# Optimization experiments

Hardware: AMD Instinct MI355X
Metric: run time of the kernel (lower is better)

## Reference

```python
import jax, jax.numpy as jnp
import numpy as np

L, H, M, KB = 8, 512, 32, 256  # layers, hidden, fourier modes, key bits
EPS = 1e-5


def setup_inputs() -> dict:
    key = jax.random.key(0)
    ks = jax.random.split(key, 20)
    B, S = 8, 2048
    s = 0.02
    return {
        'x': jax.random.normal(ks[0], (B, S), jnp.float32),
        # input projection Linear(1, H): weight [H] (squeezed), bias [H]
        'in_w': jax.random.normal(ks[1], (H,), jnp.float32) * s,
        'in_b': jax.random.normal(ks[2], (H,), jnp.float32) * s,
        # per-layer fourier weights (complex, stored as real/imag), conv1d(k=1), layernorm
        'fw_r': jax.random.normal(ks[3], (L, M, H, H), jnp.float32) * s,
        'fw_i': jax.random.normal(ks[4], (L, M, H, H), jnp.float32) * s,
        'conv_w': jax.random.normal(ks[5], (L, H, H), jnp.float32) / np.sqrt(H),
        'conv_b': jax.random.normal(ks[6], (L, H), jnp.float32) * s,
        'ln_g': jnp.ones((L, H), jnp.float32),
        'ln_b': jnp.zeros((L, H), jnp.float32),
        # output projection H -> H/2 -> H/4 -> 1
        'op1_w': jax.random.normal(ks[7], (H // 2, H), jnp.float32) / np.sqrt(H),
        'op1_b': jnp.zeros((H // 2,), jnp.float32),
        'op2_w': jax.random.normal(ks[8], (H // 4, H // 2), jnp.float32) / np.sqrt(H // 2),
        'op2_b': jnp.zeros((H // 4,), jnp.float32),
        'op3_w': jax.random.normal(ks[9], (1, H // 4), jnp.float32) / np.sqrt(H // 4),
        'op3_b': jnp.zeros((1,), jnp.float32),
        # cryptanalytic head H -> H -> KB (sigmoid)
        'h1_w': jax.random.normal(ks[10], (H, H), jnp.float32) / np.sqrt(H),
        'h1_b': jnp.zeros((H,), jnp.float32),
        'h2_w': jax.random.normal(ks[11], (KB, H), jnp.float32) / np.sqrt(H),
        'h2_b': jnp.zeros((KB,), jnp.float32),
    }


def _gelu(x):
    return jax.nn.gelu(x, approximate=False)


def _fourier_layer(x, Wc, cw, cb, g, b):
    # x: [B, S, H]; Wc: [M, H, H] complex
    S = x.shape[1]
    x_ft = jnp.fft.rfft(x, axis=1)  # [B, F, H] complex, F = S//2+1
    m = min(M, x_ft.shape[1])
    # batched per-mode complex GEMM (replaces python loop over modes)
    spec = jnp.einsum('bmh,mhk->bmk', x_ft[:, :m], Wc[:m])
    out_ft = jnp.concatenate([spec, jnp.zeros_like(x_ft[:, m:])], axis=1)
    x_fourier = jnp.fft.irfft(out_ft, n=S, axis=1)  # real [B, S, H]
    x_conv = x @ cw.T + cb  # Conv1d kernel-size-1 == per-position linear
    y = x_fourier + x_conv
    mu = jnp.mean(y, axis=-1, keepdims=True)
    var = jnp.var(y, axis=-1, keepdims=True)
    return (y - mu) * jax.lax.rsqrt(var + EPS) * g + b


def reference(x, in_w, in_b, fw_r, fw_i, conv_w, conv_b, ln_g, ln_b,
              op1_w, op1_b, op2_w, op2_b, op3_w, op3_b,
              h1_w, h1_b, h2_w, h2_b):
    # input projection: Linear(1, H) on x[..., None]
    h = x[:, :, None] * in_w[None, None, :] + in_b  # [B, S, H]
    Wc = fw_r + 1j * fw_i  # [L, M, H, H]
    for l in range(L):
        h = _fourier_layer(h, Wc[l], conv_w[l], conv_b[l], ln_g[l], ln_b[l]) + h
    # output projection (dropout is identity in eval)
    o = _gelu(h @ op1_w.T + op1_b)
    o = _gelu(o @ op2_w.T + op2_b)
    output = (o @ op3_w.T + op3_b)[..., 0]  # [B, S]
    gf = jnp.mean(h, axis=1)  # [B, H]
    k = _gelu(gf @ h1_w.T + h1_b)
    key_pred = jax.nn.sigmoid(k @ h2_w.T + h2_b)  # [B, KB]
    return output, key_pred
```

## Files before the change

### kernel.cpp

```cpp
#include <hip/hip_runtime.h>
#include <hip/hip_bf16.h>
#include <math.h>

#define BB   8
#define SEQ  2048
#define HD   512
#define LAY  8
#define MD   32
#define NKB  256
#define LNEPS 1e-5f

typedef __attribute__((ext_vector_type(8))) short v8s;
typedef __attribute__((ext_vector_type(4))) float v4f;
typedef __attribute__((ext_vector_type(4))) unsigned short v4us;

__device__ __forceinline__ float b2f(__hip_bfloat16 v) { return __bfloat162float(v); }
__device__ __forceinline__ float geluf(float v) { return v * 0.5f * (1.f + erff(v * 0.70710678118654752f)); }
__device__ __forceinline__ float bflo(unsigned int u) { return __uint_as_float((u & 0xFFFFu) << 16); }
__device__ __forceinline__ float bfhi(unsigned int u) { return __uint_as_float(u & 0xFFFF0000u); }

__device__ __forceinline__ float ldin(const void* p, size_t i, int bf) {
    if (bf) return __bfloat162float(((const __hip_bfloat16*)p)[i]);
    return ((const float*)p)[i];
}
__device__ __forceinline__ void stout(void* p, size_t i, float v, int bf) {
    if (bf) ((__hip_bfloat16*)p)[i] = __float2bfloat16(v);
    else    ((float*)p)[i] = v;
}

__device__ __forceinline__ void gl2lds16(const void* g, void* l) {
    __builtin_amdgcn_global_load_lds((__attribute__((address_space(1))) void*)g,
                                     (__attribute__((address_space(3))) void*)l, 16, 0, 0);
}

__device__ __forceinline__ unsigned short f2bfu(float f) {
    __hip_bfloat16 b = __float2bfloat16(f);
    return *(unsigned short*)&b;
}

__global__ void k_flag(const unsigned int* __restrict__ lng_bits, int* __restrict__ flag) {
    if (threadIdx.x == 0 && blockIdx.x == 0)
        *flag = (lng_bits[0] == 0x3F803F80u) ? 1 : 0;
}

__global__ void k_setup(const void* __restrict__ x, const void* __restrict__ in_w, const void* __restrict__ in_b,
                        const void* __restrict__ cw, const void* __restrict__ w1, const void* __restrict__ w2,
                        const void* __restrict__ h1w, const void* __restrict__ h2w,
                        __hip_bfloat16* __restrict__ Ffwd, __hip_bfloat16* __restrict__ T2,
                        __hip_bfloat16* __restrict__ cwbf, __hip_bfloat16* __restrict__ w1bf,
                        __hip_bfloat16* __restrict__ w2bf, float* __restrict__ h1T, float* __restrict__ h2T,
                        float* __restrict__ h,
                        float* __restrict__ gf,
                        const int* __restrict__ flag) {
    int bf = *flag;
    int blk = blockIdx.x, t = threadIdx.x;
    if (blk < 512) {
        int idx = blk * 256 + t;
        int j = idx >> 11, s = idx & 2047;
        int m = j >> 1;
        int phase = (m * s) & (SEQ - 1);
        float ang = (float)phase * (6.283185307179586f / (float)SEQ);
        Ffwd[idx] = __float2bfloat16((j & 1) ? -sinf(ang) : cosf(ang));
    } else if (blk < 1024) {
        int idx = (blk - 512) * 256 + t;
        int s = idx >> 6, j = idx & 63;
        int m = j >> 1;
        float v;
        if (j == 0)      v = 1.f / (float)SEQ;
        else if (j == 1) v = 0.f;
        else {
            int phase = (m * s) & (SEQ - 1);
            float ang = (float)phase * (6.283185307179586f / (float)SEQ);
            v = (j & 1) ? (-2.f / (float)SEQ) * sinf(ang) : (2.f / (float)SEQ) * cosf(ang);
        }
        T2[idx] = __float2bfloat16(v);
    } else if (blk < 9216) {
        int idx = (blk - 1024) * 256 + t;
        cwbf[idx] = __float2bfloat16(ldin(cw, idx, bf));
    } else if (blk < 9728) {
        int idx = (blk - 9216) * 256 + t;
        w1bf[idx] = __float2bfloat16(ldin(w1, idx, bf));
    } else if (blk < 9856) {
        int idx = (blk - 9728) * 256 + t;
        w2bf[idx] = __float2bfloat16(ldin(w2, idx, bf));
    } else if (blk < 10880) {
        int idx = (blk - 9856) * 256 + t;
        int r = idx & 511, c = idx >> 9;
        h1T[idx] = ldin(h1w, (size_t)r * 512 + c, bf);
    } else if (blk < 11392) {
        int idx = (blk - 10880) * 256 + t;
        int r = idx & 255, c = idx >> 8;
        h2T[idx] = ldin(h2w, (size_t)r * 512 + c, bf);
    } else if (blk < 11408) {
        int idx = (blk - 11392) * 256 + t;
        gf[idx] = 0.f;
    } else {
        int idx = (blk - 11408) * 256 + t;
        int j = idx & 511;
        int bs = idx >> 9;
        float v = ldin(x, bs, bf) * ldin(in_w, j, bf) + ldin(in_b, j, bf);
        h[idx] = v;
    }
}

__global__ __launch_bounds__(256) void k_fdft2(const float* __restrict__ h,
                                               const __hip_bfloat16* __restrict__ Ffwd,
                                               float* __restrict__ Xpart) {
    __shared__ __align__(16) __hip_bfloat16 Als[2][16 * 72];
    int t = threadIdx.x;
    int lane = t & 63, wv = t >> 6;
    int ln15 = lane & 15, quad = lane >> 4;
    int ht = blockIdx.x, b = blockIdx.y, kh = blockIdx.z;
    int kcs = kh * 16;
    int sr = t >> 2, hc = (t & 3) * 4;

    v4f acc = (v4f){0.f, 0.f, 0.f, 0.f};

    const float* asrc0 = h + (size_t)b * SEQ * HD + ht * 16;
    const __hip_bfloat16* fbase = Ffwd + (size_t)(wv * 16 + ln15) * SEQ + quad * 8;

    float4 cur = *(const float4*)(asrc0 + (size_t)(kcs * 64 + sr) * HD + hc);
    {
        const float* cf = (const float*)&cur;
#pragma unroll
        for (int e = 0; e < 4; e++)
            Als[0][(hc + e) * 72 + sr] = __float2bfloat16(cf[e]);
    }
    __syncthreads();
    for (int i = 0; i < 16; i++) {
        int buf = i & 1;
        float4 nxt = cur;
        if (i < 15)
            nxt = *(const float4*)(asrc0 + (size_t)((kcs + i + 1) * 64 + sr) * HD + hc);
        v8s bf0 = *(const v8s*)(fbase + (kcs + i) * 64);
        v8s bf1 = *(const v8s*)(fbase + (kcs + i) * 64 + 32);
        v8s af0 = *(const v8s*)&Als[buf][ln15 * 72 + quad * 8];
        v8s af1 = *(const v8s*)&Als[buf][ln15 * 72 + 32 + quad * 8];
        acc = __builtin_amdgcn_mfma_f32_16x16x32_bf16(af0, bf0, acc, 0, 0, 0);
        acc = __builtin_amdgcn_mfma_f32_16x16x32_bf16(af1, bf1, acc, 0, 0, 0);
        if (i < 15) {
            const float* nf = (const float*)&nxt;
#pragma unroll
            for (int e = 0; e < 4; e++)
                Als[buf ^ 1][(hc + e) * 72 + sr] = __float2bfloat16(nf[e]);
        }
        __syncthreads();
        cur = nxt;
    }
    int j = wv * 16 + ln15;
    int m = j >> 1, c = j & 1;
    int hg = ht * 16 + quad * 4;
    float* outp = Xpart + (size_t)kh * 262144 + (size_t)(b * 32 + m) * 1024;
#pragma unroll
    for (int r = 0; r < 4; r++)
        outp[(size_t)(hg + r) * 2 + c] = acc[r];
}

__global__ __launch_bounds__(512) void k_mix(const float* __restrict__ Xp0, const float* __restrict__ Xp1,
                                             const void* __restrict__ fwr, const void* __restrict__ fwi,
                                             __hip_bfloat16* __restrict__ spec2, int l,
                                             const int* __restrict__ flag) {
    int bf = *flag;
    int kt = blockIdx.x;
    int m  = blockIdx.y;
    int t = threadIdx.x;
    int kl = t & 15, hg = t >> 4;
    int k0 = kt * 64 + kl * 4;
    __shared__ float xs[8192];
    __shared__ float red[32 * 512];
    for (int e = t; e < 8192; e += 512) {
        int bb = e >> 10, r = e & 1023;
        size_t off = (size_t)(bb * 32 + m) * 1024 + r;
        xs[bb * 1024 + r] = Xp0[off] + Xp1[off];
    }
    __syncthreads();
    float ar[8][4], ai[8][4];
#pragma unroll
    for (int bb = 0; bb < 8; bb++)
#pragma unroll
        for (int q = 0; q < 4; q++) { ar[bb][q] = 0.f; ai[bb][q] = 0.f; }
    size_t wbase = (size_t)(l * 32 + m) * 262144 + k0;
    const float2* xs2 = (const float2*)xs;
    if (bf) {
        const __hip_bfloat16* fr = (const __hip_bfloat16*)fwr;
        const __hip_bfloat16* fi = (const __hip_bfloat16*)fwi;
#pragma unroll 2
        for (int hh = hg; hh < 512; hh += 32) {
            v4us urv = *(const v4us*)(fr + wbase + (size_t)hh * 512);
            v4us uiv = *(const v4us*)(fi + wbase + (size_t)hh * 512);
            float wr[4], wi[4];
#pragma unroll
            for (int q = 0; q < 4; q++) {
                wr[q] = __uint_as_float(((unsigned int)(unsigned short)urv[q]) << 16);
                wi[q] = __uint_as_float(((unsigned int)(unsigned short)uiv[q]) << 16);
            }
#pragma unroll
            for (int bb = 0; bb < 8; bb++) {
                float2 x2 = xs2[bb * 512 + hh];
#pragma unroll
                for (int q = 0; q < 4; q++) {
                    ar[bb][q] += x2.x * wr[q] - x2.y * wi[q];
                    ai[bb][q] += x2.x * wi[q] + x2.y * wr[q];
                }
            }
        }
    } else {
        const float* fr = (const float*)fwr;
        const float* fi = (const float*)fwi;
#pragma unroll 2
        for (int hh = hg; hh < 512; hh += 32) {
            v4f wrv = *(const v4f*)(fr + wbase + (size_t)hh * 512);
            v4f wiv = *(const v4f*)(fi + wbase + (size_t)hh * 512);
#pragma unroll
            for (int bb = 0; bb < 8; bb++) {
                float2 x2 = xs2[bb * 512 + hh];
#pragma unroll
                for (int q = 0; q < 4; q++) {
                    ar[bb][q] += x2.x * wrv[q] - x2.y * wiv[q];
                    ai[bb][q] += x2.x * wiv[q] + x2.y * wrv[q];
                }
            }
        }
    }
    v4f* red4 = (v4f*)red;
#pragma unroll
    for (int bb = 0; bb < 8; bb++)
        red4[hg * 128 + bb * 16 + kl] = (v4f){ar[bb][0], ar[bb][1], ar[bb][2], ar[bb][3]};
    __syncthreads();
    float sr = 0.f;
#pragma unroll
    for (int g = 0; g < 32; g++) sr += red[g * 512 + t];
    __syncthreads();
#pragma unroll
    for (int bb = 0; bb < 8; bb++)
        red4[hg * 128 + bb * 16 + kl] = (v4f){ai[bb][0], ai[bb][1], ai[bb][2], ai[bb][3]};
    __syncthreads();
    float si = 0.f;
#pragma unroll
    for (int g = 0; g < 32; g++) si += red[g * 512 + t];

    int bb = t >> 6, j = t & 63;
    int k = kt * 64 + j;
    size_t o = ((size_t)(bb * 512 + k) << 6) + 2 * m;
    __hip_bfloat16 hr = __float2bfloat16(sr), hi = __float2bfloat16(si);
    unsigned int pk = (unsigned int)*(unsigned short*)&hr | ((unsigned int)*(unsigned short*)&hi << 16);
    *(unsigned int*)(spec2 + o) = pk;
}

__global__ __launch_bounds__(512) void k_gln(__hip_bfloat16* __restrict__ hbf,
                                             const __hip_bfloat16* __restrict__ cwbf,
                                             const __hip_bfloat16* __restrict__ T2,
                                             const __hip_bfloat16* __restrict__ spec2,
                                             const void* __restrict__ cb,
                                             const void* __restrict__ lng, const void* __restrict__ lnb,
                                             float* __restrict__ h,
                                             int l, const int* __restrict__ flag) {
    int bfv = *flag;
    __shared__ __align__(16) __hip_bfloat16 smem[2][19456];
    __shared__ float stats[128];
    __hip_bfloat16* Yls = &smem[0][0];

    int t = threadIdx.x;
    int lane = t & 63, wv = t >> 6;
    int wr = wv >> 2, wc = wv & 3;
    int ln15 = lane & 15, quad = lane >> 4;
    int row0 = blockIdx.x * 64;
    int b = row0 >> 11, s0 = row0 & 2047;
    int arow = t >> 3, acolq = (t & 7) * 4;

    v4f acc[16];
#pragma unroll
    for (int i = 0; i < 16; i++) acc[i] = (v4f){0.f, 0.f, 0.f, 0.f};

    const __hip_bfloat16* cwl = cwbf + (size_t)l * 262144;

    auto stageB = [&](int buf, int kc) {
        int k0 = kc * 32;
#pragma unroll
        for (int p = 0; p < 4; p++) {
            int i = p * 512 + t;
            int n = i >> 2, kq = (i & 3) * 8;
            const __hip_bfloat16* bsrc = (k0 < 512)
                ? cwl + (size_t)n * 512 + k0 + kq
                : spec2 + (size_t)(b * 512 + n) * 64 + (k0 - 512) + kq;
            gl2lds16(bsrc, &smem[buf][2560 + (size_t)(p * 512 + wv * 64) * 8]);
        }
    };
    auto loadA = [&](int kc, float4& av, v4us& tv) {
        int k0 = kc * 32;
        if (k0 < 512) {
            av = *(const float4*)&h[(size_t)(row0 + arow) * HD + k0 + acolq];
        } else {
            tv = *(const v4us*)&T2[(size_t)(s0 + arow) * 64 + (k0 - 512) + acolq];
        }
    };
    auto writeA = [&](int buf, int kc, const float4& av, const v4us& tv) {
        __hip_bfloat16* dst = &smem[buf][arow * 40 + acolq];
        if (kc * 32 < 512) {
            const float* af = (const float*)&av;
            v4us pk;
#pragma unroll
            for (int e = 0; e < 4; e++) pk[e] = (short)f2bfu(af[e]);
            *(v4us*)dst = pk;
        } else {
            *(v4us*)dst = tv;
        }
    };

    {
        float4 av; v4us tv;
        loadA(0, av, tv);
        stageB(0, 0);
        writeA(0, 0, av, tv);
    }
    __syncthreads();
    int cur = 0;
    float4 avn; v4us tvn;
    for (int kc = 0; kc < 18; kc++) {
        if (kc < 17) {
            loadA(kc + 1, avn, tvn);
            stageB(cur ^ 1, kc + 1);
        }
        const __hip_bfloat16* Als = &smem[cur][0];
        const __hip_bfloat16* Bls = &smem[cur][2560];
        v8s af[2], bfr[8];
#pragma unroll
        for (int i = 0; i < 2; i++)
            af[i] = *(const v8s*)&Als[(wr * 32 + i * 16 + ln15) * 40 + quad * 8];
#pragma unroll
        for (int j = 0; j < 8; j++)
            bfr[j] = *(const v8s*)&Bls[(wc * 128 + j * 16 + ln15) * 32 + quad * 8];
#pragma unroll
        for (int i = 0; i < 2; i++)
#pragma unroll
            for (int j = 0; j < 8; j++)
                acc[i * 8 + j] = __builtin_amdgcn_mfma_f32_16x16x32_bf16(af[i], bfr[j], acc[i * 8 + j], 0, 0, 0);
        if (kc < 17) writeA(cur ^ 1, kc + 1, avn, tvn);
        __syncthreads();
        cur ^= 1;
    }
#pragma unroll
    for (int j = 0; j < 8; j++) {
        int col = wc * 128 + j * 16 + ln15;
        float cbv = ldin(cb, l * HD + col, bfv);
#pragma unroll
        for (int i = 0; i < 2; i++) {
            int rl = wr * 32 + i * 16 + quad * 4;
#pragma unroll
            for (int r = 0; r < 4; r++)
                Yls[(rl + r) * 520 + col] = __float2bfloat16(acc[i * 8 + j][r] + cbv);
        }
    }
    __syncthreads();
    {
        int r = t >> 3, g2 = t & 7;
        float s = 0.f, q = 0.f;
        for (int i = 0; i < 32; i++) {
            int cp = g2 + i * 8;
            unsigned int u = *(const unsigned int*)&Yls[r * 520 + cp * 2];
            float v0 = bflo(u), v1 = bfhi(u);
            s += v0 + v1; q += v0 * v0 + v1 * v1;
        }
        s += __shfl_xor(s, 1); s += __shfl_xor(s, 2); s += __shfl_xor(s, 4);
        q += __shfl_xor(q, 1); q += __shfl_xor(q, 2); q += __shfl_xor(q, 4);
        if (g2 == 0) {
            float mu = s * (1.f / (float)HD);
            float var = q * (1.f / (float)HD) - mu * mu;
            stats[r * 2] = mu; stats[r * 2 + 1] = rsqrtf(var + LNEPS);
        }
    }
    __syncthreads();
    {
        int c2 = t & 255;
        int gc = 2 * c2;
        float g0 = ldin(lng, l * HD + gc, bfv),     g1 = ldin(lng, l * HD + gc + 1, bfv);
        float b0 = ldin(lnb, l * HD + gc, bfv),     b1 = ldin(lnb, l * HD + gc + 1, bfv);
        int rbase = t >> 8;
        int last = (l == LAY - 1);
        for (int k = 0; k < 32; k++) {
            int r = rbase + 2 * k;
            float mu = stats[r * 2], rs = stats[r * 2 + 1];
            unsigned int u = *(const unsigned int*)&Yls[r * 520 + c2 * 2];
            float v0 = bflo(u), v1 = bfhi(u);
            float2 hv = *(const float2*)&h[(size_t)(row0 + r) * HD + gc];
            float n0 = (v0 - mu) * rs * g0 + b0 + hv.x;
            float n1 = (v1 - mu) * rs * g1 + b1 + hv.y;
            *(float2*)&h[(size_t)(row0 + r) * HD + gc] = (float2){n0, n1};
            if (last) {
                unsigned int up = ((unsigned int)f2bfu(n1) << 16) | (unsigned int)f2bfu(n0);
                ((unsigned int*)(hbf + (size_t)(row0 + r) * HD))[c2] = up;
            }
        }
    }
}

__global__ __launch_bounds__(256) void k_pj1(const __hip_bfloat16* __restrict__ hbf,
                                             const __hip_bfloat16* __restrict__ w1bf,
                                             const void* __restrict__ b1,
                                             __hip_bfloat16* __restrict__ o1bf,
                                             const int* __restrict__ flag) {
    int bfv = *flag;
    __shared__ __align__(16) __hip_bfloat16 smem[2][8192];
    int t = threadIdx.x;
    int lane = t & 63, wv = t >> 6;
    int wr = wv >> 1, wc = wv & 1;
    int ln15 = lane & 15, quad = lane >> 4;
    int row0 = blockIdx.x * 128, n0 = blockIdx.y * 128;

    v4f acc[16];
#pragma unroll
    for (int i = 0; i < 16; i++) acc[i] = (v4f){0.f, 0.f, 0.f, 0.f};

    auto stage = [&](int buf, int kc) {
        int k0 = kc * 32;
#pragma unroll
        for (int p = 0; p < 2; p++) {
            int i = p * 256 + t;
            int row = i >> 2, kq = (i & 3) * 8;
            gl2lds16(hbf + (size_t)(row0 + row) * 512 + k0 + kq, &smem[buf][(size_t)(p * 256 + wv * 64) * 8]);
            gl2lds16(w1bf + (size_t)(n0 + row) * 512 + k0 + kq, &smem[buf][4096 + (size_t)(p * 256 + wv * 64) * 8]);
        }
    };

    stage(0, 0);
    __syncthreads();
    int cur = 0;
    for (int kc = 0; kc < 16; kc++) {
        if (kc < 15) stage(cur ^ 1, kc + 1);
        const __hip_bfloat16* Als = &smem[cur][0];
        const __hip_bfloat16* Bls = &smem[cur][4096];
        v8s af[4], bfr[4];
#pragma unroll
        for (int i = 0; i < 4; i++)
            af[i] = *(const v8s*)&Als[(wr * 64 + i * 16 + ln15) * 32 + quad * 8];
#pragma unroll
        for (int j = 0; j < 4; j++)
            bfr[j] = *(const v8s*)&Bls[(wc * 64 + j * 16 + ln15) * 32 + quad * 8];
#pragma unroll
        for (int i = 0; i < 4; i++)
#pragma unroll
            for (int j = 0; j < 4; j++)
                acc[i * 4 + j] = __builtin_amdgcn_mfma_f32_16x16x32_bf16(af[i], bfr[j], acc[i * 4 + j], 0, 0, 0);
        __syncthreads();
        cur ^= 1;
    }
#pragma unroll
    for (int j = 0; j < 4; j++) {
        int col = n0 + wc * 64 + j * 16 + ln15;
        float bv = ldin(b1, col, bfv);
#pragma unroll
        for (int i = 0; i < 4; i++) {
            int rg = row0 + wr * 64 + i * 16 + quad * 4;
#pragma unroll
            for (int r = 0; r < 4; r++)
                o1bf[(size_t)(rg + r) * 256 + col] = __float2bfloat16(geluf(acc[i * 4 + j][r] + bv));
        }
    }
}

__global__ __launch_bounds__(256) void k_pj2(const __hip_bfloat16* __restrict__ o1bf,
                                             const __hip_bfloat16* __restrict__ w2bf,
                                             const void* __restrict__ b2,
                                             const void* __restrict__ w3, const void* __restrict__ b3,
                                             void* __restrict__ out, const int* __restrict__ flag) {
    int bfv = *flag;
    __shared__ __align__(16) __hip_bfloat16 smem[2][8192];
    __shared__ __hip_bfloat16 o2s[128 * 130];
    __shared__ float w3s[128];
    int t = threadIdx.x;
    int lane = t & 63, wv = t >> 6;
    int wr = wv >> 1, wc = wv & 1;
    int ln15 = lane & 15, quad = lane >> 4;
    int row0 = blockIdx.x * 128;
    if (t < 128) w3s[t] = ldin(w3, t, bfv);

    v4f acc[16];
#pragma unroll
    for (int i = 0; i < 16; i++) acc[i] = (v4f){0.f, 0.f, 0.f, 0.f};

    auto stage = [&](int buf, int kc) {
        int k0 = kc * 32;
#pragma unroll
        for (int p = 0; p < 2; p++) {
            int i = p * 256 + t;
            int row = i >> 2, kq = (i & 3) * 8;
            gl2lds16(o1bf + (size_t)(row0 + row) * 256 + k0 + kq, &smem[buf][(size_t)(p * 256 + wv * 64) * 8]);
            gl2lds16(w2bf + (size_t)row * 256 + k0 + kq,          &smem[buf][4096 + (size_t)(p * 256 + wv * 64) * 8]);
        }
    };

    stage(0, 0);
    __syncthreads();
    int cur = 0;
    for (int kc = 0; kc < 8; kc++) {
        if (kc < 7) stage(cur ^ 1, kc + 1);
        const __hip_bfloat16* Als = &smem[cur][0];
        const __hip_bfloat16* Bls = &smem[cur][4096];
        v8s af[4], bfr[4];
#pragma unroll
        for (int i = 0; i < 4; i++)
            af[i] = *(const v8s*)&Als[(wr * 64 + i * 16 + ln15) * 32 + quad * 8];
#pragma unroll
        for (int j = 0; j < 4; j++)
            bfr[j] = *(const v8s*)&Bls[(wc * 64 + j * 16 + ln15) * 32 + quad * 8];
#pragma unroll
        for (int i = 0; i < 4; i++)
#pragma unroll
            for (int j = 0; j < 4; j++)
                acc[i * 4 + j] = __builtin_amdgcn_mfma_f32_16x16x32_bf16(af[i], bfr[j], acc[i * 4 + j], 0, 0, 0);
        __syncthreads();
        cur ^= 1;
    }
#pragma unroll
    for (int j = 0; j < 4; j++) {
        int col = wc * 64 + j * 16 + ln15;
        float bv = ldin(b2, col, bfv);
#pragma unroll
        for (int i = 0; i < 4; i++) {
            int rl = wr * 64 + i * 16 + quad * 4;
#pragma unroll
            for (int r = 0; r < 4; r++)
                o2s[(rl + r) * 130 + col] = __float2bfloat16(geluf(acc[i * 4 + j][r] + bv));
        }
    }
    __syncthreads();
    if (t < 128) {
        float s = 0.f;
        for (int j = 0; j < 128; j++) s += b2f(o2s[t * 130 + j]) * w3s[j];
        stout(out, row0 + t, s + ldin(b3, 0, bfv), bfv);
    }
}

__global__ __launch_bounds__(512) void k_gf(const float* __restrict__ h, float* __restrict__ gf) {
    int sc = blockIdx.x, b = blockIdx.y;
    int j = threadIdx.x;
    const float* p = h + ((size_t)b * SEQ + sc * 64) * HD + j;
    float s = 0.f;
    for (int i = 0; i < 64; i++) s += p[(size_t)i * HD];
    atomicAdd(&gf[b * HD + j], s * (1.f / (float)SEQ));
}

__global__ __launch_bounds__(512) void k_head(const float* __restrict__ gf,
                                              const float* __restrict__ h1T, const void* __restrict__ h1b,
                                              const float* __restrict__ h2T, const void* __restrict__ h2b,
                                              void* __restrict__ out, const int* __restrict__ flag) {
    int bf = *flag;
    int b = blockIdx.x;
    int t = threadIdx.x;
    __shared__ float gs[512];
    __shared__ float ks[512];
    gs[t] = gf[b * HD + t];
    __syncthreads();
    float a = 0.f;
    for (int j = 0; j < 512; j++) a += gs[j] * h1T[j * 512 + t];
    ks[t] = geluf(a + ldin(h1b, t, bf));
    __syncthreads();
    if (t < 256) {
        float s = 0.f;
        for (int j = 0; j < 512; j++) s += ks[j] * h2T[j * 256 + t];
        s += ldin(h2b, t, bf);
        stout(out, BB * SEQ + b * NKB + t, 1.f / (1.f + expf(-s)), bf);
    }
}

extern "C" void kernel_launch(void* const* d_in, const int* in_sizes, int n_in,
                              void* d_out, int out_size, void* d_ws, size_t ws_size,
                              hipStream_t stream) {
    const void* x    = d_in[0];
    const void* in_w = d_in[1];
    const void* in_b = d_in[2];
    const void* fwr  = d_in[3];
    const void* fwi  = d_in[4];
    const void* cw   = d_in[5];
    const void* cb   = d_in[6];
    const void* lng  = d_in[7];
    const void* lnb  = d_in[8];
    const void* w1   = d_in[9];
    const void* b1   = d_in[10];
    const void* w2   = d_in[11];
    const void* b2   = d_in[12];
    const void* w3   = d_in[13];
    const void* b3   = d_in[14];
    const void* h1w  = d_in[15];
    const void* h1b  = d_in[16];
    const void* h2w  = d_in[17];
    const void* h2b  = d_in[18];

    float* ws = (float*)d_ws;
    __hip_bfloat16* Ffwd = (__hip_bfloat16*)ws;
    float*          h    = ws + 131072;
    float*          Xp   = h + 8388608;
    __hip_bfloat16* o1bf = (__hip_bfloat16*)Xp;
    __hip_bfloat16* hbf  = (__hip_bfloat16*)(Xp + 4194304);
    __hip_bfloat16* cwbf = (__hip_bfloat16*)(Xp + 8388608);
    __hip_bfloat16* T2   = (__hip_bfloat16*)(Xp + 10485760);
    __hip_bfloat16* spec2= (__hip_bfloat16*)(Xp + 10551296);
    float*          XftOld = Xp + 10682368;
    float*          gf   = XftOld + 262144;
    float*          w1T  = gf + 4096;
    __hip_bfloat16* w1bf = (__hip_bfloat16*)w1T;
    __hip_bfloat16* w2bf = (__hip_bfloat16*)(w1T + 65536);
    float*          w2T  = w1T + 131072;
    float*          h1T  = w2T + 32768;
    float*          h2T  = h1T + 262144;
    int*            flag = (int*)(h2T + 131072);
    float*          Xpart = h2T + 131072 + 64;

    k_flag<<<1, 1, 0, stream>>>((const unsigned int*)lng, flag);
    k_setup<<<44176, 256, 0, stream>>>(x, in_w, in_b, cw, w1, w2, h1w, h2w,
                                       Ffwd, T2, cwbf, w1bf, w2bf, h1T, h2T,
                                       h, gf, flag);

    for (int l = 0; l < LAY; l++) {
        k_fdft2<<<dim3(32, 8, 2), 256, 0, stream>>>(h, Ffwd, Xpart);
        k_mix<<<dim3(8, 32), 512, 0, stream>>>(Xpart, Xpart + 262144, fwr, fwi, spec2, l, flag);
        k_gln<<<256, 512, 0, stream>>>(hbf, cwbf, T2, spec2, cb, lng, lnb, h, l, flag);
    }

    k_gf<<<dim3(32, 8), 512, 0, stream>>>(h, gf);
    k_pj1<<<dim3(128, 2), 256, 0, stream>>>(hbf, w1bf, b1, o1bf, flag);
    k_pj2<<<128, 256, 0, stream>>>(o1bf, w2bf, b2, w3, b3, d_out, flag);
    k_head<<<8, 512, 0, stream>>>(gf, h1T, h1b, h2T, h2b, d_out, flag);
}
```

Before: 1.167 ms.

## Split Fourier mode mixing into split-K partial kernel plus reduction kernel

Replaces the single mode-mixing kernel (256 blocks, in-block shared-memory reduction over 32 h-groups) with a split-K scheme: 512 blocks each cover 32 input channels for all 512 outputs and write float2 partials to global memory, and a second kernel sums the 16 partials and packs them to bf16. The aim is more parallelism and coalesced per-thread weight loads for streaming the large complex weight tensor, and to drop the large shared reduction buffer so occupancy can rise. The cost is an extra launch per layer and about 2 MB of partial-sum global traffic per layer.

```diff
diff --git a/kernel.cpp b/kernel.cpp
--- a/kernel.cpp
+++ b/kernel.cpp
@@ -156,92 +156,74 @@
         outp[(size_t)(hg + r) * 2 + c] = acc[r];
 }
 
-__global__ __launch_bounds__(512) void k_mix(const float* __restrict__ Xp0, const float* __restrict__ Xp1,
-                                             const void* __restrict__ fwr, const void* __restrict__ fwi,
-                                             __hip_bfloat16* __restrict__ spec2, int l,
-                                             const int* __restrict__ flag) {
+__global__ __launch_bounds__(512) void k_mixp(const float* __restrict__ Xp0, const float* __restrict__ Xp1,
+                                              const void* __restrict__ fwr, const void* __restrict__ fwi,
+                                              float* __restrict__ Ppart, int l,
+                                              const int* __restrict__ flag) {
     int bf = *flag;
-    int kt = blockIdx.x;
+    int ht = blockIdx.x;
     int m  = blockIdx.y;
-    int t = threadIdx.x;
-    int kl = t & 15, hg = t >> 4;
-    int k0 = kt * 64 + kl * 4;
+    int t  = threadIdx.x;
     __shared__ float xs[8192];
-    __shared__ float red[32 * 512];
     for (int e = t; e < 8192; e += 512) {
         int bb = e >> 10, r = e & 1023;
         size_t off = (size_t)(bb * 32 + m) * 1024 + r;
-        xs[bb * 1024 + r] = Xp0[off] + Xp1[off];
-    }
-    __syncthreads();
-    float ar[8][4], ai[8][4];
-#pragma unroll
-    for (int bb = 0; bb < 8; bb++)
-#pragma unroll
-        for (int q = 0; q < 4; q++) { ar[bb][q] = 0.f; ai[bb][q] = 0.f; }
-    size_t wbase = (size_t)(l * 32 + m) * 262144 + k0;
+        xs[e] = Xp0[off] + Xp1[off];
+    }
+    __syncthreads();
+    float ar[8], ai[8];
+#pragma unroll
+    for (int bb = 0; bb < 8; bb++) { ar[bb] = 0.f; ai[bb] = 0.f; }
+    size_t wbase = (size_t)(l * 32 + m) * 262144;
     const float2* xs2 = (const float2*)xs;
+    int h0 = ht * 32;
     if (bf) {
         const __hip_bfloat16* fr = (const __hip_bfloat16*)fwr;
         const __hip_bfloat16* fi = (const __hip_bfloat16*)fwi;
-#pragma unroll 2
-        for (int hh = hg; hh < 512; hh += 32) {
-            v4us urv = *(const v4us*)(fr + wbase + (size_t)hh * 512);
-            v4us uiv = *(const v4us*)(fi + wbase + (size_t)hh * 512);
-            float wr[4], wi[4];
-#pragma unroll
-            for (int q = 0; q < 4; q++) {
-                wr[q] = __uint_as_float(((unsigned int)(unsigned short)urv[q]) << 16);
-                wi[q] = __uint_as_float(((unsigned int)(unsigned short)uiv[q]) << 16);
-            }
+#pragma unroll 4
+        for (int hh = h0; hh < h0 + 32; hh++) {
+            float wr = b2f(fr[wbase + (size_t)hh * 512 + t]);
+            float wi = b2f(fi[wbase + (size_t)hh * 512 + t]);
 #pragma unroll
             for (int bb = 0; bb < 8; bb++) {
                 float2 x2 = xs2[bb * 512 + hh];
-#pragma unroll
-                for (int q = 0; q < 4; q++) {
-                    ar[bb][q] += x2.x * wr[q] - x2.y * wi[q];
-                    ai[bb][q] += x2.x * wi[q] + x2.y * wr[q];
-                }
+                ar[bb] += x2.x * wr - x2.y * wi;
+                ai[bb] += x2.x * wi + x2.y * wr;
             }
         }
     } else {
         const float* fr = (const float*)fwr;
         const float* fi = (const float*)fwi;
-#pragma unroll 2
-        for (int hh = hg; hh < 512; hh += 32) {
-            v4f wrv = *(const v4f*)(fr + wbase + (size_t)hh * 512);
-            v4f wiv = *(const v4f*)(fi + wbase + (size_t)hh * 512);
+#pragma unroll 4
+        for (int hh = h0; hh < h0 + 32; hh++) {
+            float wr = fr[wbase + (size_t)hh * 512 + t];
+            float wi = fi[wbase + (size_t)hh * 512 + t];
 #pragma unroll
             for (int bb = 0; bb < 8; bb++) {
                 float2 x2 = xs2[bb * 512 + hh];
-#pragma unroll
-                for (int q = 0; q < 4; q++) {
-                    ar[bb][q] += x2.x * wrv[q] - x2.y * wiv[q];
-                    ai[bb][q] += x2.x * wiv[q] + x2.y * wrv[q];
-                }
+                ar[bb] += x2.x * wr - x2.y * wi;
+                ai[bb] += x2.x * wi + x2.y * wr;
             }
         }
     }
-    v4f* red4 = (v4f*)red;
+    float2* pp = (float2*)Ppart;
 #pragma unroll
     for (int bb = 0; bb < 8; bb++)
-        red4[hg * 128 + bb * 16 + kl] = (v4f){ar[bb][0], ar[bb][1], ar[bb][2], ar[bb][3]};
-    __syncthreads();
-    float sr = 0.f;
-#pragma unroll
-    for (int g = 0; g < 32; g++) sr += red[g * 512 + t];
-    __syncthreads();
-#pragma unroll
-    for (int bb = 0; bb < 8; bb++)
-        red4[hg * 128 + bb * 16 + kl] = (v4f){ai[bb][0], ai[bb][1], ai[bb][2], ai[bb][3]};
-    __syncthreads();
-    float si = 0.f;
-#pragma unroll
-    for (int g = 0; g < 32; g++) si += red[g * 512 + t];
-
-    int bb = t >> 6, j = t & 63;
-    int k = kt * 64 + j;
-    size_t o = ((size_t)(bb * 512 + k) << 6) + 2 * m;
+        pp[((size_t)(m * 16 + ht) * 8 + bb) * 512 + t] = (float2){ar[bb], ai[bb]};
+}
+
+__global__ __launch_bounds__(256) void k_mixr(const float* __restrict__ Ppart,
+                                              __hip_bfloat16* __restrict__ spec2) {
+    int g = blockIdx.x * 256 + threadIdx.x;
+    int k = g & 511, b = (g >> 9) & 7, m = g >> 12;
+    const float2* pp = (const float2*)Ppart;
+    float sr = 0.f, si = 0.f;
+#pragma unroll
+    for (int ht = 0; ht < 16; ht++) {
+        float2 v = pp[((size_t)(m * 16 + ht) * 8 + b) * 512 + k];
+        sr += v.x; si += v.y;
+    }
+    size_t o = ((size_t)(b * 512 + k) << 6) + 2 * m;
     __hip_bfloat16 hr = __float2bfloat16(sr), hi = __float2bfloat16(si);
     unsigned int pk = (unsigned int)*(unsigned short*)&hr | ((unsigned int)*(unsigned short*)&hi << 16);
     *(unsigned int*)(spec2 + o) = pk;
@@ -605,6 +587,7 @@
     float*          h2T  = h1T + 262144;
     int*            flag = (int*)(h2T + 131072);
     float*          Xpart = h2T + 131072 + 64;
+    float*          Ppart = Xpart + 524288;
 
     k_flag<<<1, 1, 0, stream>>>((const unsigned int*)lng, flag);
     k_setup<<<44176, 256, 0, stream>>>(x, in_w, in_b, cw, w1, w2, h1w, h2w,
@@ -613,7 +596,8 @@
 
     for (int l = 0; l < LAY; l++) {
         k_fdft2<<<dim3(32, 8, 2), 256, 0, stream>>>(h, Ffwd, Xpart);
-        k_mix<<<dim3(8, 32), 512, 0, stream>>>(Xpart, Xpart + 262144, fwr, fwi, spec2, l, flag);
+        k_mixp<<<dim3(16, 32), 512, 0, stream>>>(Xpart, Xpart + 262144, fwr, fwi, Ppart, l, flag);
+        k_mixr<<<512, 256, 0, stream>>>(Ppart, spec2);
         k_gln<<<256, 512, 0, stream>>>(hbf, cwbf, T2, spec2, cb, lng, lnb, h, l, flag);
     }
 
```

New measurement: 1.140 ms. 2.3% less time.
